# Kernel optimization log

Measured on AMD Instinct MI355X. Metric: run time of the kernel, lower is better.

## Reference

```python
import jax, jax.numpy as jnp
import numpy as np

VOCAB = 32000; DIM = 512; NL = 6; B = 2; L = 1024
DI = 2 * DIM      # d_inner (expand=2)
DS = 16           # d_state
DC = 4            # d_conv
DR = DIM // 16    # dt_rank = ceil(512/16) = 32


def setup_inputs() -> dict:
    key = jax.random.key(0)
    ks = jax.random.split(key, 10)
    s = 0.02
    tokens = jax.random.randint(ks[0], (B, L), 0, VOCAB)
    pos_emb = jax.random.normal(ks[1], (1, L, DIM)) * s
    embed = jax.random.normal(ks[2], (VOCAB, DIM)) * s
    lm_w = jax.random.normal(ks[3], (VOCAB, DIM)) * s
    lm_b = jnp.zeros((VOCAB,), jnp.float32)
    in_proj_w = jax.random.normal(ks[4], (NL, 2 * DI, DIM)) * s
    conv_w = jax.random.normal(ks[5], (NL, DI, DC)) * s
    conv_b = jnp.zeros((NL, DI), jnp.float32)
    x_proj_w = jax.random.normal(ks[6], (NL, DR + 2 * DS, DI)) * s
    dt_proj_w = jax.random.normal(ks[7], (NL, DI, DR)) * s
    dt_proj_b = jnp.broadcast_to(jnp.log(jnp.expm1(jnp.float32(0.01))), (NL, DI)).astype(jnp.float32)
    A_log = jnp.log(jnp.broadcast_to(jnp.arange(1, DS + 1, dtype=jnp.float32), (NL, DI, DS)))
    Dp = jnp.ones((NL, DI), jnp.float32)
    out_w = jax.random.normal(ks[8], (NL, DIM, DI)) * s
    ln_g = jnp.ones((NL, DIM), jnp.float32)
    ln_b = jnp.zeros((NL, DIM), jnp.float32)
    return dict(tokens=tokens, pos_emb=pos_emb, embed=embed, lm_w=lm_w, lm_b=lm_b,
                in_proj_w=in_proj_w, conv_w=conv_w, conv_b=conv_b, x_proj_w=x_proj_w,
                dt_proj_w=dt_proj_w, dt_proj_b=dt_proj_b, A_log=A_log, Dp=Dp,
                out_w=out_w, ln_g=ln_g, ln_b=ln_b)


def silu(x):
    return x * jax.nn.sigmoid(x)


def layernorm(x, g, b, eps=1e-5):
    mu = jnp.mean(x, -1, keepdims=True)
    var = jnp.var(x, -1, keepdims=True)
    return (x - mu) * jax.lax.rsqrt(var + eps) * g + b


def causal_dwconv(x, w, b):
    # x: (B,L,DI), w: (DI,DC) depthwise, left-pad causal
    xp = jnp.pad(x, ((0, 0), (DC - 1, 0), (0, 0)))
    y = b
    for k in range(DC):
        y = y + w[:, k] * xp[:, k:k + x.shape[1], :]
    return y


def selective_scan(u, dt, A, Bm, Cm, Dp):
    # u,dt: (B,L,DI); A: (DI,DS); Bm,Cm: (B,L,DS)
    dA = jnp.exp(dt[..., None] * A)                       # (B,L,DI,DS)
    dBu = dt[..., None] * Bm[:, :, None, :] * u[..., None]
    h0 = jnp.zeros((u.shape[0], DI, DS), u.dtype)

    def step(h, inp):
        dA_t, dBu_t, C_t = inp
        h = dA_t * h + dBu_t
        y = jnp.einsum('bdn,bn->bd', h, C_t)
        return h, y

    _, ys = jax.lax.scan(step, h0, (dA.transpose(1, 0, 2, 3),
                                    dBu.transpose(1, 0, 2, 3),
                                    Cm.transpose(1, 0, 2)))
    return ys.transpose(1, 0, 2) + u * Dp


def mamba_block(x, in_w, cw, cb, xp_w, dtw, dtb, A_log, Dp, ow):
    xz = jnp.einsum('bld,ed->ble', x, in_w)               # (B,L,2*DI)
    xc, z = jnp.split(xz, 2, axis=-1)
    xc = silu(causal_dwconv(xc, cw, cb))
    x_dbl = jnp.einsum('bld,ed->ble', xc, xp_w)           # (B,L,DR+2*DS)
    dt, Bm, Cm = jnp.split(x_dbl, [DR, DR + DS], axis=-1)
    dt = jax.nn.softplus(jnp.einsum('blr,dr->bld', dt, dtw) + dtb)
    A = -jnp.exp(A_log)
    y = selective_scan(xc, dt, A, Bm, Cm, Dp)
    y = y * silu(z)
    return jnp.einsum('bld,ed->ble', y, ow)


def reference(tokens, pos_emb, embed, lm_w, lm_b, in_proj_w, conv_w, conv_b,
              x_proj_w, dt_proj_w, dt_proj_b, A_log, Dp, out_w, ln_g, ln_b):
    x = embed[tokens] + pos_emb[:, :tokens.shape[1]]
    for i in range(NL):
        res = x
        x = mamba_block(x, in_proj_w[i], conv_w[i], conv_b[i], x_proj_w[i],
                        dt_proj_w[i], dt_proj_b[i], A_log[i], Dp[i], out_w[i])
        x = layernorm(x + res, ln_g[i], ln_b[i])
    return jnp.einsum('bld,vd->blv', x, lm_w) + lm_b
```

## Files before the change

kernel.cpp:

```cpp
#include <hip/hip_runtime.h>
#include <hip/hip_bf16.h>
#include <math.h>

#define BB 2
#define LL 1024
#define DIM 512
#define NL 6
#define DI 1024
#define DS 16
#define DC 4
#define DR 32
#define VOCAB 32000
#define M_ROWS (BB * LL)
#define CCH 32
#define CHLEN (LL / CCH)
#define KSPLIT 8

typedef unsigned short u16;
typedef __attribute__((ext_vector_type(8))) short bf16x8;
typedef __attribute__((ext_vector_type(4))) float f32x4;

__device__ __forceinline__ u16 f2bf(float f) {
    unsigned u = __float_as_uint(f);
    u += 0x7FFF + ((u >> 16) & 1);
    return (u16)(u >> 16);
}
#define SWZ(r, c) ((c) ^ (((r) >> 1) & 3))

__global__ __launch_bounds__(256) void cast_bf16(const float* __restrict__ in,
                                                 u16* __restrict__ out, int n8) {
    int idx = blockIdx.x * 256 + threadIdx.x;
    if (idx >= n8) return;
    float4 v0 = ((const float4*)in)[idx * 2];
    float4 v1 = ((const float4*)in)[idx * 2 + 1];
    union { u16 h[8]; int4 v; } r;
    r.h[0] = f2bf(v0.x); r.h[1] = f2bf(v0.y); r.h[2] = f2bf(v0.z); r.h[3] = f2bf(v0.w);
    r.h[4] = f2bf(v1.x); r.h[5] = f2bf(v1.y); r.h[6] = f2bf(v1.z); r.h[7] = f2bf(v1.w);
    ((int4*)out)[idx] = r.v;
}

__global__ __launch_bounds__(256) void embed_kernel(const int* __restrict__ tok,
                                                    const float* __restrict__ pos,
                                                    const float* __restrict__ emb,
                                                    float* __restrict__ x,
                                                    u16* __restrict__ xb) {
    int idx = blockIdx.x * 256 + threadIdx.x;
    int d = idx & (DIM - 1);
    int l = (idx >> 9) & (LL - 1);
    int b = idx >> 19;
    int t = tok[b * LL + l];
    float v = emb[(size_t)t * DIM + d] + pos[l * DIM + d];
    x[idx] = v;
    xb[idx] = f2bf(v);
}

__global__ __launch_bounds__(256) void gemm_bf16(const u16* __restrict__ A,
                                                 const u16* __restrict__ W,
                                                 const float* __restrict__ bias,
                                                 float* __restrict__ C,
                                                 int M, int N, int K,
                                                 int lda, int ldw, int mode) {
    __shared__ __align__(16) u16 As[128 * 32];
    __shared__ __align__(16) u16 Ws[128 * 32];
    const int t = threadIdx.x;
    const int l = t & 63;
    const int w = t >> 6;
    const int nwg = gridDim.x;
    const int q = nwg >> 3, r8 = nwg & 7;
    const int xcd = blockIdx.x & 7, rank = blockIdx.x >> 3;
    const int wgid = (xcd < r8 ? xcd * (q + 1) : r8 * (q + 1) + (xcd - r8) * q) + rank;
    const int Mb = M >> 7;
    const int bm = (wgid % Mb) * 128;
    const int bn = (wgid / Mb) * 128;
    const int wm = (w >> 1) * 64;
    const int wn = (w & 1) * 64;

    f32x4 acc[4][4] = {};

    for (int k0 = 0; k0 < K; k0 += 32) {
#pragma unroll
        for (int p = 0; p < 2; ++p) {
            const int i = (p * 4 + w) * 64 + l;
            const int row = i >> 2;
            const int kq = SWZ(row, i & 3);
            __builtin_amdgcn_global_load_lds(
                (const __attribute__((address_space(1))) unsigned int*)
                    (A + (size_t)(bm + row) * lda + k0 + kq * 8),
                (__attribute__((address_space(3))) unsigned int*)
                    (As + (p * 4 + w) * 512),
                16, 0, 0);
            __builtin_amdgcn_global_load_lds(
                (const __attribute__((address_space(1))) unsigned int*)
                    (W + (size_t)(bn + row) * ldw + k0 + kq * 8),
                (__attribute__((address_space(3))) unsigned int*)
                    (Ws + (p * 4 + w) * 512),
                16, 0, 0);
        }
        asm volatile("s_waitcnt vmcnt(0)" ::: "memory");
        __syncthreads();
#pragma unroll
        for (int mi = 0; mi < 4; ++mi) {
            const int ar = wm + mi * 16 + (l & 15);
            bf16x8 a = *(const bf16x8*)(As + ar * 32 + SWZ(ar, l >> 4) * 8);
#pragma unroll
            for (int ni = 0; ni < 4; ++ni) {
                const int wr = wn + ni * 16 + (l & 15);
                bf16x8 b = *(const bf16x8*)(Ws + wr * 32 + SWZ(wr, l >> 4) * 8);
                acc[mi][ni] = __builtin_amdgcn_mfma_f32_16x16x32_bf16(b, a, acc[mi][ni], 0, 0, 0);
            }
        }
        __syncthreads();
    }

#pragma unroll
    for (int mi = 0; mi < 4; ++mi) {
        const int row = bm + wm + mi * 16 + (l & 15);
#pragma unroll
        for (int ni = 0; ni < 4; ++ni) {
            const int col = bn + wn + ni * 16 + ((l >> 4) << 2);
            float4 v;
            v.x = acc[mi][ni][0]; v.y = acc[mi][ni][1];
            v.z = acc[mi][ni][2]; v.w = acc[mi][ni][3];
            if (bias != nullptr) {
                float4 b4 = *(const float4*)(bias + col);
                v.x += b4.x; v.y += b4.y; v.z += b4.z; v.w += b4.w;
            }
            if (mode == 1) {
                v.x = (v.x > 20.f) ? v.x : log1pf(__expf(v.x));
                v.y = (v.y > 20.f) ? v.y : log1pf(__expf(v.y));
                v.z = (v.z > 20.f) ? v.z : log1pf(__expf(v.z));
                v.w = (v.w > 20.f) ? v.w : log1pf(__expf(v.w));
            }
            *(float4*)(C + (size_t)row * N + col) = v;
        }
    }
}

__global__ __launch_bounds__(256) void gemm_n64(const u16* __restrict__ A,
                                                const u16* __restrict__ W,
                                                float* __restrict__ out,
                                                int lda, int ldw, int ldc,
                                                int KS, int pstride) {
    __shared__ __align__(16) u16 As[128 * 32];
    __shared__ __align__(16) u16 Ws[64 * 32];
    const int t = threadIdx.x;
    const int l = t & 63;
    const int w = t >> 6;
    const int kz = blockIdx.x;
    const int bm = blockIdx.y * 128;
    const int bnn = blockIdx.z * 64;
    const int wm = w * 32;

    f32x4 acc[2][4] = {};

    const int kbeg = kz * KS;
    for (int k0 = kbeg; k0 < kbeg + KS; k0 += 32) {
#pragma unroll
        for (int p = 0; p < 2; ++p) {
            const int i = p * 256 + w * 64 + l;
            const int row = i >> 2;
            const int kq = SWZ(row, i & 3);
            __builtin_amdgcn_global_load_lds(
                (const __attribute__((address_space(1))) unsigned int*)
                    (A + (size_t)(bm + row) * lda + k0 + kq * 8),
                (__attribute__((address_space(3))) unsigned int*)
                    (As + (p * 256 + w * 64) * 8),
                16, 0, 0);
        }
        {
            const int i = w * 64 + l;
            const int row = i >> 2;
            const int kq = SWZ(row, i & 3);
            __builtin_amdgcn_global_load_lds(
                (const __attribute__((address_space(1))) unsigned int*)
                    (W + (size_t)(bnn + row) * ldw + k0 + kq * 8),
                (__attribute__((address_space(3))) unsigned int*)
                    (Ws + (w * 64) * 8),
                16, 0, 0);
        }
        asm volatile("s_waitcnt vmcnt(0)" ::: "memory");
        __syncthreads();
#pragma unroll
        for (int mi = 0; mi < 2; ++mi) {
            const int ar = wm + mi * 16 + (l & 15);
            bf16x8 a = *(const bf16x8*)(As + ar * 32 + SWZ(ar, l >> 4) * 8);
#pragma unroll
            for (int ni = 0; ni < 4; ++ni) {
                const int wr = ni * 16 + (l & 15);
                bf16x8 b = *(const bf16x8*)(Ws + wr * 32 + SWZ(wr, l >> 4) * 8);
                acc[mi][ni] = __builtin_amdgcn_mfma_f32_16x16x32_bf16(b, a, acc[mi][ni], 0, 0, 0);
            }
        }
        __syncthreads();
    }

    float* op = out + (size_t)kz * pstride;
#pragma unroll
    for (int mi = 0; mi < 2; ++mi) {
        const int row = bm + wm + mi * 16 + (l & 15);
#pragma unroll
        for (int ni = 0; ni < 4; ++ni) {
            const int col = bnn + ni * 16 + ((l >> 4) << 2);
            float4 v;
            v.x = acc[mi][ni][0]; v.y = acc[mi][ni][1];
            v.z = acc[mi][ni][2]; v.w = acc[mi][ni][3];
            *(float4*)(op + (size_t)row * ldc + col) = v;
        }
    }
}

__global__ __launch_bounds__(256) void xdreduce(const float* __restrict__ Pf,
                                                float* __restrict__ xd,
                                                u16* __restrict__ xdb) {
    int idx = blockIdx.x * 256 + threadIdx.x;
    float s = 0.f;
#pragma unroll
    for (int kz = 0; kz < KSPLIT; ++kz)
        s += Pf[(size_t)kz * (M_ROWS * 64) + idx];
    xd[idx] = s;
    xdb[idx] = f2bf(s);
}

__global__ __launch_bounds__(256) void conv_silu(const float* __restrict__ xz,
                                                 const float* __restrict__ cw,
                                                 const float* __restrict__ cb,
                                                 float* __restrict__ xc,
                                                 u16* __restrict__ xcb) {
    int idx = blockIdx.x * 256 + threadIdx.x;
    int c = idx & (DI - 1);
    int l = (idx >> 10) & (LL - 1);
    int b = idx >> 20;
    float acc = cb[c];
#pragma unroll
    for (int k = 0; k < DC; ++k) {
        int ll = l + k - (DC - 1);
        if (ll >= 0)
            acc += cw[c * DC + k] * xz[((size_t)(b * LL + ll)) * (2 * DI) + c];
    }
    float v = acc / (1.f + __expf(-acc));
    xc[idx] = v;
    xcb[idx] = f2bf(v);
}

__global__ __launch_bounds__(256) void scan_pass1(const float* __restrict__ xc,
                                                  const float* __restrict__ dt,
                                                  const float* __restrict__ xdbl,
                                                  const float* __restrict__ A_log,
                                                  float* __restrict__ S,
                                                  float* __restrict__ Q) {
    const int d = blockIdx.x * 256 + threadIdx.x;
    const int b = blockIdx.y;
    const int c = blockIdx.z;
    float a[DS];
#pragma unroll
    for (int q = 0; q < 4; ++q) {
        float4 al = *(const float4*)(A_log + d * DS + q * 4);
        a[q * 4 + 0] = -__expf(al.x);
        a[q * 4 + 1] = -__expf(al.y);
        a[q * 4 + 2] = -__expf(al.z);
        a[q * 4 + 3] = -__expf(al.w);
    }
    float Qr[DS];
#pragma unroll
    for (int n = 0; n < DS; ++n) Qr[n] = 0.f;
    float Ssum = 0.f;

    const int l0 = c * CHLEN;
    const float* dtp = dt + ((size_t)b * LL + l0) * DI + d;
    const float* up  = xc + ((size_t)b * LL + l0) * DI + d;
    const float* xdp = xdbl + ((size_t)b * LL + l0) * 64 + DR;

    for (int l = 0; l < CHLEN; ++l) {
        float dtv = dtp[(size_t)l * DI];
        float uv  = up[(size_t)l * DI];
        float wv = dtv * uv;
        Ssum += dtv;
#pragma unroll
        for (int q = 0; q < 4; ++q) {
            float4 Bv = *(const float4*)(xdp + l * 64 + q * 4);
            float dA0 = __expf(dtv * a[q * 4 + 0]);
            float dA1 = __expf(dtv * a[q * 4 + 1]);
            float dA2 = __expf(dtv * a[q * 4 + 2]);
            float dA3 = __expf(dtv * a[q * 4 + 3]);
            Qr[q * 4 + 0] = dA0 * Qr[q * 4 + 0] + wv * Bv.x;
            Qr[q * 4 + 1] = dA1 * Qr[q * 4 + 1] + wv * Bv.y;
            Qr[q * 4 + 2] = dA2 * Qr[q * 4 + 2] + wv * Bv.z;
            Qr[q * 4 + 3] = dA3 * Qr[q * 4 + 3] + wv * Bv.w;
        }
    }
    S[((size_t)b * CCH + c) * DI + d] = Ssum;
    float* Qp = Q + (((size_t)b * CCH + c) * DI + d) * DS;
#pragma unroll
    for (int q = 0; q < 4; ++q) {
        float4 o;
        o.x = Qr[q * 4 + 0]; o.y = Qr[q * 4 + 1];
        o.z = Qr[q * 4 + 2]; o.w = Qr[q * 4 + 3];
        *(float4*)(Qp + q * 4) = o;
    }
}

__global__ __launch_bounds__(256) void scan_pass2(const float* __restrict__ A_log,
                                                  const float* __restrict__ S,
                                                  float* __restrict__ Q) {
    const int idx = blockIdx.x * 256 + threadIdx.x;
    const int b = idx >> 14;
    const int dn = idx & 16383;
    const int d = dn >> 4;
    const float a = -__expf(A_log[dn]);
    float h = 0.f;
    for (int c = 0; c < CCH; ++c) {
        const size_t soff = ((size_t)b * CCH + c) * DI + d;
        const size_t qoff = ((size_t)b * CCH + c) * (size_t)(DI * DS) + dn;
        float P = __expf(a * S[soff]);
        float qv = Q[qoff];
        Q[qoff] = h;
        h = P * h + qv;
    }
}

__global__ __launch_bounds__(256) void scan_pass3(const float* __restrict__ xc,
                                                  const float* __restrict__ dt,
                                                  const float* __restrict__ xdbl,
                                                  const float* __restrict__ xz,
                                                  const float* __restrict__ A_log,
                                                  const float* __restrict__ Dpp,
                                                  const float* __restrict__ Q,
                                                  u16* __restrict__ y) {
    const int d = blockIdx.x * 256 + threadIdx.x;
    const int b = blockIdx.y;
    const int c = blockIdx.z;
    float a[DS];
#pragma unroll
    for (int q = 0; q < 4; ++q) {
        float4 al = *(const float4*)(A_log + d * DS + q * 4);
        a[q * 4 + 0] = -__expf(al.x);
        a[q * 4 + 1] = -__expf(al.y);
        a[q * 4 + 2] = -__expf(al.z);
        a[q * 4 + 3] = -__expf(al.w);
    }
    float h[DS];
    const float* Qp = Q + (((size_t)b * CCH + c) * DI + d) * DS;
#pragma unroll
    for (int q = 0; q < 4; ++q) {
        float4 hv = *(const float4*)(Qp + q * 4);
        h[q * 4 + 0] = hv.x; h[q * 4 + 1] = hv.y;
        h[q * 4 + 2] = hv.z; h[q * 4 + 3] = hv.w;
    }
    const float dp = Dpp[d];

    const int l0 = c * CHLEN;
    const float* dtp = dt + ((size_t)b * LL + l0) * DI + d;
    const float* up  = xc + ((size_t)b * LL + l0) * DI + d;
    const float* xdp = xdbl + ((size_t)b * LL + l0) * 64 + DR;
    const float* zp  = xz + ((size_t)b * LL + l0) * (2 * DI) + DI + d;
    u16* yp = y + ((size_t)b * LL + l0) * DI + d;

    for (int l = 0; l < CHLEN; ++l) {
        float dtv = dtp[(size_t)l * DI];
        float uv  = up[(size_t)l * DI];
        float wv = dtv * uv;
        float p = 0.f;
#pragma unroll
        for (int q = 0; q < 4; ++q) {
            float4 Bv = *(const float4*)(xdp + l * 64 + q * 4);
            float4 Cv = *(const float4*)(xdp + l * 64 + 16 + q * 4);
            float dA0 = __expf(dtv * a[q * 4 + 0]);
            float dA1 = __expf(dtv * a[q * 4 + 1]);
            float dA2 = __expf(dtv * a[q * 4 + 2]);
            float dA3 = __expf(dtv * a[q * 4 + 3]);
            h[q * 4 + 0] = dA0 * h[q * 4 + 0] + wv * Bv.x;
            h[q * 4 + 1] = dA1 * h[q * 4 + 1] + wv * Bv.y;
            h[q * 4 + 2] = dA2 * h[q * 4 + 2] + wv * Bv.z;
            h[q * 4 + 3] = dA3 * h[q * 4 + 3] + wv * Bv.w;
            p += h[q * 4 + 0] * Cv.x + h[q * 4 + 1] * Cv.y +
                 h[q * 4 + 2] * Cv.z + h[q * 4 + 3] * Cv.w;
        }
        float zv = zp[(size_t)l * (2 * DI)];
        float g = zv / (1.f + __expf(-zv));
        yp[(size_t)l * DI] = f2bf((p + uv * dp) * g);
    }
}

__global__ __launch_bounds__(256) void add_ln(const float* __restrict__ o,
                                              float* __restrict__ x,
                                              const float* __restrict__ g,
                                              const float* __restrict__ b,
                                              u16* __restrict__ xb) {
    int m = blockIdx.x;
    int t = threadIdx.x;
    const float* xr = x + (size_t)m * DIM;
    const float* orr = o + (size_t)m * DIM;
    float v0 = xr[t] + orr[t];
    float v1 = xr[t + 256] + orr[t + 256];
    float s = v0 + v1;
    float ss = v0 * v0 + v1 * v1;
#pragma unroll
    for (int off = 32; off > 0; off >>= 1) {
        s += __shfl_down(s, off, 64);
        ss += __shfl_down(ss, off, 64);
    }
    __shared__ float sb[4], ssb[4];
    int w = t >> 6;
    if ((t & 63) == 0) { sb[w] = s; ssb[w] = ss; }
    __syncthreads();
    float stot = sb[0] + sb[1] + sb[2] + sb[3];
    float sstot = ssb[0] + ssb[1] + ssb[2] + ssb[3];
    float mean = stot * (1.f / DIM);
    float var = sstot * (1.f / DIM) - mean * mean;
    float rs = rsqrtf(var + 1e-5f);
    float* xw = x + (size_t)m * DIM;
    float o0 = (v0 - mean) * rs * g[t] + b[t];
    float o1 = (v1 - mean) * rs * g[t + 256] + b[t + 256];
    xw[t] = o0;
    xw[t + 256] = o1;
    xb[(size_t)m * DIM + t] = f2bf(o0);
    xb[(size_t)m * DIM + t + 256] = f2bf(o1);
}

extern "C" void kernel_launch(void* const* d_in, const int* in_sizes, int n_in,
                              void* d_out, int out_size, void* d_ws, size_t ws_size,
                              hipStream_t stream) {
    const int*   tokens = (const int*)d_in[0];
    const float* pos    = (const float*)d_in[1];
    const float* emb    = (const float*)d_in[2];
    const float* lm_w   = (const float*)d_in[3];
    const float* lm_b   = (const float*)d_in[4];
    const float* in_w   = (const float*)d_in[5];
    const float* cw     = (const float*)d_in[6];
    const float* cb     = (const float*)d_in[7];
    const float* xpw    = (const float*)d_in[8];
    const float* dtw    = (const float*)d_in[9];
    const float* dtb    = (const float*)d_in[10];
    const float* A_log  = (const float*)d_in[11];
    const float* Dpp    = (const float*)d_in[12];
    const float* ow     = (const float*)d_in[13];
    const float* lng    = (const float*)d_in[14];
    const float* lnb    = (const float*)d_in[15];
    float* out = (float*)d_out;

    float* ws = (float*)d_ws;
    float* x    = ws;
    float* xz   = x + 1048576;
    float* xc   = xz + 4194304;
    float* xd   = xc + 2097152;
    float* dt   = xd + 131072;
    float* o    = dt + 2097152;
    float* S    = o + 1048576;
    float* Qb   = S + 65536;
    float* Pf   = Qb + 1048576;
    u16* xb     = (u16*)(Pf + 1048576);
    u16* yb     = xb + 1048576;
    u16* xcb    = yb + 2097152;
    u16* xdb    = xcb + 2097152;
    u16* lm_wb  = xdb + 131072;
    u16* in_wb  = lm_wb + 16384000;
    u16* owb    = in_wb + 6291456;
    u16* xpwb   = owb + 3145728;
    u16* dtwb   = xpwb + 393216;

    cast_bf16<<<16384000 / 8 / 256, 256, 0, stream>>>(lm_w, lm_wb, 16384000 / 8);
    cast_bf16<<<6291456 / 8 / 256, 256, 0, stream>>>(in_w, in_wb, 6291456 / 8);
    cast_bf16<<<3145728 / 8 / 256, 256, 0, stream>>>(ow, owb, 3145728 / 8);
    cast_bf16<<<393216 / 8 / 256, 256, 0, stream>>>(xpw, xpwb, 393216 / 8);
    cast_bf16<<<196608 / 8 / 256, 256, 0, stream>>>(dtw, dtwb, 196608 / 8);

    embed_kernel<<<M_ROWS * DIM / 256, 256, 0, stream>>>(tokens, pos, emb, x, xb);

    for (int i = 0; i < NL; ++i) {
        gemm_bf16<<<(2048 / 128) * (M_ROWS / 128), 256, 0, stream>>>(
            xb, in_wb + (size_t)i * 2048 * 512, nullptr, xz,
            M_ROWS, 2048, 512, 512, 512, 0);
        conv_silu<<<M_ROWS * DI / 256, 256, 0, stream>>>(
            xz, cw + (size_t)i * DI * DC, cb + (size_t)i * DI, xc, xcb);
        gemm_n64<<<dim3(KSPLIT, M_ROWS / 128, 1), 256, 0, stream>>>(
            xcb, xpwb + (size_t)i * 64 * 1024, Pf,
            1024, 1024, 64, 1024 / KSPLIT, M_ROWS * 64);
        xdreduce<<<M_ROWS * 64 / 256, 256, 0, stream>>>(Pf, xd, xdb);
        gemm_bf16<<<(1024 / 128) * (M_ROWS / 128), 256, 0, stream>>>(
            xdb, dtwb + (size_t)i * 1024 * 32, dtb + (size_t)i * DI, dt,
            M_ROWS, 1024, 32, 64, 32, 1);
        scan_pass1<<<dim3(DI / 256, BB, CCH), 256, 0, stream>>>(
            xc, dt, xd, A_log + (size_t)i * DI * DS, S, Qb);
        scan_pass2<<<(BB * DI * DS) / 256, 256, 0, stream>>>(
            A_log + (size_t)i * DI * DS, S, Qb);
        scan_pass3<<<dim3(DI / 256, BB, CCH), 256, 0, stream>>>(
            xc, dt, xd, xz, A_log + (size_t)i * DI * DS, Dpp + (size_t)i * DI, Qb, yb);
        gemm_n64<<<dim3(1, M_ROWS / 128, 512 / 64), 256, 0, stream>>>(
            yb, owb + (size_t)i * 512 * 1024, o,
            1024, 1024, 512, 1024, 0);
        add_ln<<<M_ROWS, 256, 0, stream>>>(
            o, x, lng + (size_t)i * DIM, lnb + (size_t)i * DIM, xb);
    }

    gemm_bf16<<<(VOCAB / 128) * (M_ROWS / 128), 256, 0, stream>>>(
        xb, lm_wb, lm_b, out, M_ROWS, VOCAB, 512, 512, 512, 0);
}
```

Before: 955.4 us.

## Triple-buffer GEMM LDS tiles with async prefetch and double scan chunk count

Both bf16 GEMM kernels now keep three LDS tile buffers and issue global-to-LDS loads two tiles ahead. Partial vmcnt waits let the MFMA work on the current tile overlap with loads still in flight, instead of draining all memory and syncing twice per K step. Separately, the selective-scan chunk count goes from 32 to 64 to expose more parallelism, and the chunk-state workspace buffers are resized to match. This costs more LDS per block, which may lower occupancy, and the hand-counted waitcnt values have to match the number of loads issued per stage.

```diff
diff --git a/kernel.cpp b/kernel.cpp
--- a/kernel.cpp
+++ b/kernel.cpp
@@ -12,7 +12,7 @@
 #define DR 32
 #define VOCAB 32000
 #define M_ROWS (BB * LL)
-#define CCH 32
+#define CCH 64
 #define CHLEN (LL / CCH)
 #define KSPLIT 8
 
@@ -60,8 +60,8 @@
                                                  float* __restrict__ C,
                                                  int M, int N, int K,
                                                  int lda, int ldw, int mode) {
-    __shared__ __align__(16) u16 As[128 * 32];
-    __shared__ __align__(16) u16 Ws[128 * 32];
+    __shared__ __align__(16) u16 As[3 * 4096];
+    __shared__ __align__(16) u16 Ws[3 * 4096];
     const int t = threadIdx.x;
     const int l = t & 63;
     const int w = t >> 6;
@@ -76,8 +76,9 @@
     const int wn = (w & 1) * 64;
 
     f32x4 acc[4][4] = {};
-
-    for (int k0 = 0; k0 < K; k0 += 32) {
+    const int nt = K >> 5;
+
+    auto STAGE = [&](int bufi, int k0) {
 #pragma unroll
         for (int p = 0; p < 2; ++p) {
             const int i = (p * 4 + w) * 64 + l;
@@ -87,29 +88,53 @@
                 (const __attribute__((address_space(1))) unsigned int*)
                     (A + (size_t)(bm + row) * lda + k0 + kq * 8),
                 (__attribute__((address_space(3))) unsigned int*)
-                    (As + (p * 4 + w) * 512),
+                    (As + bufi * 4096 + (p * 4 + w) * 512),
                 16, 0, 0);
             __builtin_amdgcn_global_load_lds(
                 (const __attribute__((address_space(1))) unsigned int*)
                     (W + (size_t)(bn + row) * ldw + k0 + kq * 8),
                 (__attribute__((address_space(3))) unsigned int*)
-                    (Ws + (p * 4 + w) * 512),
+                    (Ws + bufi * 4096 + (p * 4 + w) * 512),
                 16, 0, 0);
         }
-        asm volatile("s_waitcnt vmcnt(0)" ::: "memory");
-        __syncthreads();
+    };
+    auto COMPUTE = [&](int bufi) {
+        const u16* Ab = As + bufi * 4096;
+        const u16* Wb = Ws + bufi * 4096;
 #pragma unroll
         for (int mi = 0; mi < 4; ++mi) {
             const int ar = wm + mi * 16 + (l & 15);
-            bf16x8 a = *(const bf16x8*)(As + ar * 32 + SWZ(ar, l >> 4) * 8);
+            bf16x8 a = *(const bf16x8*)(Ab + ar * 32 + SWZ(ar, l >> 4) * 8);
 #pragma unroll
             for (int ni = 0; ni < 4; ++ni) {
                 const int wr = wn + ni * 16 + (l & 15);
-                bf16x8 b = *(const bf16x8*)(Ws + wr * 32 + SWZ(wr, l >> 4) * 8);
+                bf16x8 b = *(const bf16x8*)(Wb + wr * 32 + SWZ(wr, l >> 4) * 8);
                 acc[mi][ni] = __builtin_amdgcn_mfma_f32_16x16x32_bf16(b, a, acc[mi][ni], 0, 0, 0);
             }
         }
-        __syncthreads();
+    };
+
+    STAGE(0, 0);
+    if (nt == 1) {
+        asm volatile("s_waitcnt vmcnt(0)\ns_barrier" ::: "memory");
+        COMPUTE(0);
+    } else {
+        STAGE(1, 32);
+        int b0 = 0;
+        for (int tt = 0; tt < nt - 2; ++tt) {
+            int b2 = b0 + 2; if (b2 >= 3) b2 -= 3;
+            STAGE(b2, (tt + 2) << 5);
+            asm volatile("s_waitcnt vmcnt(8)\ns_barrier" ::: "memory");
+            COMPUTE(b0);
+            asm volatile("s_waitcnt lgkmcnt(0)\ns_barrier" ::: "memory");
+            ++b0; if (b0 == 3) b0 = 0;
+        }
+        asm volatile("s_waitcnt vmcnt(4)\ns_barrier" ::: "memory");
+        COMPUTE(b0);
+        asm volatile("s_waitcnt lgkmcnt(0)\ns_barrier" ::: "memory");
+        ++b0; if (b0 == 3) b0 = 0;
+        asm volatile("s_waitcnt vmcnt(0)\ns_barrier" ::: "memory");
+        COMPUTE(b0);
     }
 
 #pragma unroll
@@ -141,8 +166,8 @@
                                                 float* __restrict__ out,
                                                 int lda, int ldw, int ldc,
                                                 int KS, int pstride) {
-    __shared__ __align__(16) u16 As[128 * 32];
-    __shared__ __align__(16) u16 Ws[64 * 32];
+    __shared__ __align__(16) u16 As[3 * 4096];
+    __shared__ __align__(16) u16 Ws[3 * 2048];
     const int t = threadIdx.x;
     const int l = t & 63;
     const int w = t >> 6;
@@ -152,9 +177,10 @@
     const int wm = w * 32;
 
     f32x4 acc[2][4] = {};
-
+    const int nt = KS >> 5;
     const int kbeg = kz * KS;
-    for (int k0 = kbeg; k0 < kbeg + KS; k0 += 32) {
+
+    auto STAGE = [&](int bufi, int k0) {
 #pragma unroll
         for (int p = 0; p < 2; ++p) {
             const int i = p * 256 + w * 64 + l;
@@ -164,7 +190,7 @@
                 (const __attribute__((address_space(1))) unsigned int*)
                     (A + (size_t)(bm + row) * lda + k0 + kq * 8),
                 (__attribute__((address_space(3))) unsigned int*)
-                    (As + (p * 256 + w * 64) * 8),
+                    (As + bufi * 4096 + (p * 256 + w * 64) * 8),
                 16, 0, 0);
         }
         {
@@ -175,23 +201,47 @@
                 (const __attribute__((address_space(1))) unsigned int*)
                     (W + (size_t)(bnn + row) * ldw + k0 + kq * 8),
                 (__attribute__((address_space(3))) unsigned int*)
-                    (Ws + (w * 64) * 8),
+                    (Ws + bufi * 2048 + (w * 64) * 8),
                 16, 0, 0);
         }
-        asm volatile("s_waitcnt vmcnt(0)" ::: "memory");
-        __syncthreads();
+    };
+    auto COMPUTE = [&](int bufi) {
+        const u16* Ab = As + bufi * 4096;
+        const u16* Wb = Ws + bufi * 2048;
 #pragma unroll
         for (int mi = 0; mi < 2; ++mi) {
             const int ar = wm + mi * 16 + (l & 15);
-            bf16x8 a = *(const bf16x8*)(As + ar * 32 + SWZ(ar, l >> 4) * 8);
+            bf16x8 a = *(const bf16x8*)(Ab + ar * 32 + SWZ(ar, l >> 4) * 8);
 #pragma unroll
             for (int ni = 0; ni < 4; ++ni) {
                 const int wr = ni * 16 + (l & 15);
-                bf16x8 b = *(const bf16x8*)(Ws + wr * 32 + SWZ(wr, l >> 4) * 8);
+                bf16x8 b = *(const bf16x8*)(Wb + wr * 32 + SWZ(wr, l >> 4) * 8);
                 acc[mi][ni] = __builtin_amdgcn_mfma_f32_16x16x32_bf16(b, a, acc[mi][ni], 0, 0, 0);
             }
         }
-        __syncthreads();
+    };
+
+    STAGE(0, kbeg);
+    if (nt == 1) {
+        asm volatile("s_waitcnt vmcnt(0)\ns_barrier" ::: "memory");
+        COMPUTE(0);
+    } else {
+        STAGE(1, kbeg + 32);
+        int b0 = 0;
+        for (int tt = 0; tt < nt - 2; ++tt) {
+            int b2 = b0 + 2; if (b2 >= 3) b2 -= 3;
+            STAGE(b2, kbeg + ((tt + 2) << 5));
+            asm volatile("s_waitcnt vmcnt(6)\ns_barrier" ::: "memory");
+            COMPUTE(b0);
+            asm volatile("s_waitcnt lgkmcnt(0)\ns_barrier" ::: "memory");
+            ++b0; if (b0 == 3) b0 = 0;
+        }
+        asm volatile("s_waitcnt vmcnt(3)\ns_barrier" ::: "memory");
+        COMPUTE(b0);
+        asm volatile("s_waitcnt lgkmcnt(0)\ns_barrier" ::: "memory");
+        ++b0; if (b0 == 3) b0 = 0;
+        asm volatile("s_waitcnt vmcnt(0)\ns_barrier" ::: "memory");
+        COMPUTE(b0);
     }
 
     float* op = out + (size_t)kz * pstride;
@@ -446,8 +496,8 @@
     float* dt   = xd + 131072;
     float* o    = dt + 2097152;
     float* S    = o + 1048576;
-    float* Qb   = S + 65536;
-    float* Pf   = Qb + 1048576;
+    float* Qb   = S + 131072;
+    float* Pf   = Qb + 2097152;
     u16* xb     = (u16*)(Pf + 1048576);
     u16* yb     = xb + 1048576;
     u16* xcb    = yb + 2097152;
```

After: 908.3 us. 1.05x faster.
